# Optimization experiments

Measured on AMD Instinct MI355X. Metric: run time of the kernel, lower is better.

## Reference

```python
import jax, jax.numpy as jnp
import numpy as np

B, T, E, H, D = 4, 2048, 1024, 16, 64  # batch, seq(block_size), n_embed, num_heads, hidden_dim


def setup_inputs() -> dict:
    key = jax.random.key(0)
    ks = jax.random.split(key, 10)
    s_in = 1.0 / np.sqrt(E)
    return {
        "x": jax.random.normal(ks[0], (B, T, E), dtype=jnp.float32),
        "Wq": jax.random.normal(ks[1], (H, E, D), dtype=jnp.float32) * s_in,
        "bq": jnp.zeros((H, D), dtype=jnp.float32),
        "Wk": jax.random.normal(ks[2], (H, E, D), dtype=jnp.float32) * s_in,
        "bk": jnp.zeros((H, D), dtype=jnp.float32),
        "Wv": jax.random.normal(ks[3], (H, E, D), dtype=jnp.float32) * s_in,
        "bv": jnp.zeros((H, D), dtype=jnp.float32),
        "Wp": jax.random.normal(ks[4], (E, E), dtype=jnp.float32) * s_in,
        "bp": jnp.zeros((E,), dtype=jnp.float32),
    }


def reference(x, Wq, bq, Wk, bk, Wv, bv, Wp, bp):
    # Batched equivalent of the per-head Python loop: each head h computes
    # causal scaled-dot-product attention with its own Q/K/V projections.
    q = jnp.einsum("bte,hed->bhtd", x, Wq) + bq[None, :, None, :]
    k = jnp.einsum("bte,hed->bhtd", x, Wk) + bk[None, :, None, :]
    v = jnp.einsum("bte,hed->bhtd", x, Wv) + bv[None, :, None, :]
    scale = 1.0 / jnp.sqrt(jnp.asarray(D, dtype=x.dtype))
    scores = jnp.einsum("bhtd,bhsd->bhts", q, k) * scale  # [B,H,T,T]
    causal = jnp.tril(jnp.ones((T, T), dtype=bool))
    scores = jnp.where(causal[None, None, :, :], scores, jnp.asarray(-jnp.inf, dtype=x.dtype))
    att = jax.nn.softmax(scores, axis=-1)
    head_out = jnp.einsum("bhts,bhsd->bhtd", att, v)  # [B,H,T,D]
    # concat heads along last dim: [B,T,H*D] == [B,T,E]
    cat = head_out.transpose(0, 2, 1, 3).reshape(B, T, H * D)
    out = cat @ Wp + bp  # final projection (dropout is identity in eval)
    return out
```

## Files before the change

kernel.cpp:

```cpp
#include <hip/hip_runtime.h>


typedef __attribute__((ext_vector_type(8))) __bf16 bf16x8;
typedef __attribute__((ext_vector_type(4))) float f32x4;
typedef __attribute__((ext_vector_type(16))) float f32x16;
typedef __attribute__((ext_vector_type(4))) unsigned int u32x4;
typedef __attribute__((ext_vector_type(2))) unsigned int u32x2;
typedef unsigned short u16;
typedef unsigned int u32;

#define DEV __device__ __forceinline__

#define QK_SCALE 0.18033688011112042f

DEV u16 f2bf(float f) {
  u32 u = __builtin_bit_cast(u32, f);
  u += 0x7fffu + ((u >> 16) & 1u);
  return (u16)(u >> 16);
}
DEV u32 pack2(float a, float b) { return (u32)f2bf(a) | ((u32)f2bf(b) << 16); }

DEV float exp2_hw(float x) { float r; asm("v_exp_f32 %0, %1" : "=v"(r) : "v"(x)); return r; }
DEV u32 cvtpk_bf16(float lo, float hi) {
  u32 r; asm("v_cvt_pk_bf16_f32 %0, %1, %2" : "=v"(r) : "v"(lo), "v"(hi)); return r;
}
DEV void pl32swap(u32& a, u32& b) { asm("v_permlane32_swap_b32 %0, %1" : "+v"(a), "+v"(b)); }
DEV float max3f(float a, float b, float c) {
  float r; asm("v_max3_f32 %0, %1, %2, %3" : "=v"(r) : "v"(a), "v"(b), "v"(c)); return r;
}

DEV f32x16 zero16() { f32x16 z;
#pragma unroll
  for (int i = 0; i < 16; i++) z[i] = 0.f;
  return z; }

DEV void gll16(const u16* g, u16* l) {
  __builtin_amdgcn_global_load_lds((const __attribute__((address_space(1))) void*)g,
                                   (__attribute__((address_space(3))) void*)l, 16, 0, 0);
}

__global__ __launch_bounds__(256) void prep_all_kernel(
    const float* __restrict__ x, const float* __restrict__ bq, const float* __restrict__ bk,
    const float* __restrict__ bv, const float* __restrict__ Wq, const float* __restrict__ Wk,
    const float* __restrict__ Wv, const float* __restrict__ Wp,
    u16* __restrict__ xbf, float* __restrict__ bqkv, u16* __restrict__ wqkvT, u16* __restrict__ wpT) {
  __shared__ float t[64][65];
  int bidAll = blockIdx.x, tid = threadIdx.x;
  if (bidAll < 4096) {
    int gid = bidAll * 256 + tid;
    if (gid < 3072) {
      float v = (gid < 1024) ? bq[gid] * QK_SCALE : (gid < 2048 ? bk[gid - 1024] : bv[gid - 2048]);
      bqkv[gid] = v;
    }
    const float4* xv = (const float4*)x;
    float4 f0 = xv[(size_t)gid * 2];
    float4 f1 = xv[(size_t)gid * 2 + 1];
    u32x4 st;
    st.x = pack2(f0.x, f0.y); st.y = pack2(f0.z, f0.w);
    st.z = pack2(f1.x, f1.y); st.w = pack2(f1.z, f1.w);
    *(u32x4*)&xbf[(size_t)gid * 8] = st;
    return;
  }
  int bid = bidAll - 4096;
  int r0 = tid >> 6, c = tid & 63;
  if (bid < 768) {
    int p = bid >> 8, rem = bid & 255, h = rem >> 4, et = rem & 15;
    float sc = (p == 0) ? QK_SCALE : 1.0f;
    const float* src = (p == 0 ? Wq : (p == 1 ? Wk : Wv)) + ((size_t)h * 1024 + et * 64) * 64;
#pragma unroll
    for (int i = 0; i < 16; i++) { int e = r0 + i * 4; t[e][c] = src[(size_t)e * 64 + c]; }
    __syncthreads();
    u16* dst = wqkvT + ((size_t)p * 1024 + h * 64) * 1024 + et * 64;
#pragma unroll
    for (int i = 0; i < 16; i++) { int d = r0 + i * 4; dst[(size_t)d * 1024 + c] = f2bf(t[c][d] * sc); }
  } else {
    int b2 = bid - 768, rt = b2 >> 4, ct = b2 & 15;
#pragma unroll
    for (int i = 0; i < 16; i++) { int e = r0 + i * 4; t[e][c] = Wp[(size_t)(rt * 64 + e) * 1024 + ct * 64 + c]; }
    __syncthreads();
#pragma unroll
    for (int i = 0; i < 16; i++) { int f = r0 + i * 4; wpT[(size_t)(ct * 64 + f) * 1024 + rt * 64 + c] = f2bf(t[c][f]); }
  }
}

DEV void stage_tile32(const u16* __restrict__ X, int row0, int k0, u16* lds, int tid) {
#pragma unroll
  for (int j = 0; j < 2; j++) {
    int ci = j * 256 + tid;
    int L = ci >> 3, half = (ci >> 2) & 1, s = ci & 3;
    int row = L * 2 + half;
    int srcslot = s ^ (L & 3);
    gll16(X + (size_t)(row0 + row) * 1024 + k0 + srcslot * 8, lds + ci * 8);
  }
}

DEV int frag_off32(int row, int lg) {
  return (row >> 1) * 64 + (row & 1) * 32 + ((lg ^ ((row >> 1) & 3)) * 8);
}

__global__ __launch_bounds__(256, 4) void gemm128_kernel(
    const u16* __restrict__ A, const u16* __restrict__ Bt, const float* __restrict__ bias,
    int tilesN, int mode, u16* __restrict__ Qb, u16* __restrict__ Kb, u16* __restrict__ VTb,
    float* __restrict__ outF) {
  __shared__ u16 As[2][128 * 32];
  __shared__ u16 Bs[2][128 * 32];
  int nwg = gridDim.x;
  int bid = blockIdx.x;
  int swz = (bid % 8) * (nwg / 8) + bid / 8;
  int bm = swz / tilesN, bn = swz % tilesN;
  int tid = threadIdx.x;
  int lane = tid & 63, wave = tid >> 6;
  int wm = wave >> 1, wn = wave & 1;
  int lr = lane & 15, lg = lane >> 4;

  f32x4 acc[4][4];
#pragma unroll
  for (int i = 0; i < 4; i++)
#pragma unroll
    for (int j = 0; j < 4; j++) acc[i][j] = f32x4{0.f, 0.f, 0.f, 0.f};

  int aoff[4], boff[4];
#pragma unroll
  for (int i = 0; i < 4; i++) {
    aoff[i] = frag_off32(wm * 64 + i * 16 + lr, lg);
    boff[i] = frag_off32(wn * 64 + i * 16 + lr, lg);
  }

  stage_tile32(A, bm * 128, 0, As[0], tid);
  stage_tile32(Bt, bn * 128, 0, Bs[0], tid);
  __syncthreads();
  int cur = 0;

  for (int t = 0; t < 32; ++t) {
    if (t + 1 < 32) {
      stage_tile32(A, bm * 128, (t + 1) * 32, As[cur ^ 1], tid);
      stage_tile32(Bt, bn * 128, (t + 1) * 32, Bs[cur ^ 1], tid);
    }
    bf16x8 af[4], bfr[4];
#pragma unroll
    for (int i = 0; i < 4; i++) {
      af[i] = *(const bf16x8*)&As[cur][aoff[i]];
      bfr[i] = *(const bf16x8*)&Bs[cur][boff[i]];
    }
    __builtin_amdgcn_s_setprio(1);
#pragma unroll
    for (int i = 0; i < 4; i++)
#pragma unroll
      for (int j = 0; j < 4; j++)
        acc[i][j] = __builtin_amdgcn_mfma_f32_16x16x32_bf16(af[i], bfr[j], acc[i][j], 0, 0, 0);
    __builtin_amdgcn_s_setprio(0);
    __syncthreads();
    cur ^= 1;
  }

  int crow = bm * 128 + wm * 64;
  int ccol = bn * 128 + wn * 64;
  if (mode == 0) {
#pragma unroll
    for (int j = 0; j < 4; j++) {
      int col = ccol + j * 16 + lr;
      float bb = bias[col];
      int p = col >> 10, h = (col >> 6) & 15, d = col & 63;
#pragma unroll
      for (int i = 0; i < 4; i++) {
        int row0 = crow + i * 16 + lg * 4;
        int b_ = row0 >> 11, t0 = row0 & 2047;
        if (p == 2) {
          u32x2 pv;
          pv.x = pack2(acc[i][j][0] + bb, acc[i][j][1] + bb);
          pv.y = pack2(acc[i][j][2] + bb, acc[i][j][3] + bb);
          *(u32x2*)&VTb[((size_t)(b_ * 16 + h) * 64 + d) * 2048 + t0] = pv;
        } else {
          u16* dst = (p == 0 ? Qb : Kb);
#pragma unroll
          for (int r = 0; r < 4; r++)
            dst[((size_t)(b_ * 16 + h) * 2048 + (t0 + r)) * 64 + d] = f2bf(acc[i][j][r] + bb);
        }
      }
    }
  } else {
#pragma unroll
    for (int j = 0; j < 4; j++) {
      int col = ccol + j * 16 + lr;
      float bb = bias[col];
#pragma unroll
      for (int i = 0; i < 4; i++) {
        int row0 = crow + i * 16 + lg * 4;
#pragma unroll
        for (int r = 0; r < 4; r++)
          outF[(size_t)(row0 + r) * 1024 + col] = acc[i][j][r] + bb;
      }
    }
  }
}

DEV void stage_kv256(const u16* __restrict__ Kh, const u16* __restrict__ Vh, int kv0,
                     u16* Ksb, u16* Vsb, int tid) {
#pragma unroll
  for (int j = 0; j < 2; j++) {
    int ci = j * 256 + tid;
    int row = ci >> 3, slot = ci & 7;
    int ss = slot ^ (row & 7);
    __builtin_amdgcn_global_load_lds(
        (const __attribute__((address_space(1))) void*)(Kh + (size_t)(kv0 + row) * 64 + ss * 8),
        (__attribute__((address_space(3))) void*)(Ksb + ci * 8), 16, 0, 0);
    __builtin_amdgcn_global_load_lds(
        (const __attribute__((address_space(1))) void*)(Vh + (size_t)row * 2048 + kv0 + ss * 8),
        (__attribute__((address_space(3))) void*)(Vsb + ci * 8), 16, 0, 0);
  }
}

__global__ __launch_bounds__(256, 2) void attn_kernel(
    const u16* __restrict__ Qb, const u16* __restrict__ Kb, const u16* __restrict__ VTb,
    u16* __restrict__ cat) {
  __shared__ u16 Ks[2][64 * 64];
  __shared__ u16 Vs[2][64 * 64];
  int bid = blockIdx.x;
  int t = 15 - (bid >> 6);
  int bh = bid & 63;
  int b = bh >> 4, h = bh & 15;
  int tid = threadIdx.x, wave = tid >> 6, lane = tid & 63;
  int l31 = lane & 31, hi = lane >> 5;
  int q0w = t * 128 + wave * 32;
  int qrow = q0w + l31;

  const u16* Qh = Qb + (size_t)bh * 2048 * 64;
  const u16* Kh = Kb + (size_t)bh * 2048 * 64;
  const u16* Vh = VTb + (size_t)bh * 64 * 2048;

  bf16x8 qf[4];
#pragma unroll
  for (int ks = 0; ks < 4; ks++)
    qf[ks] = *(const bf16x8*)&Qh[(size_t)qrow * 64 + ks * 16 + hi * 8];

  u32 loff[4];
#pragma unroll
  for (int ks = 0; ks < 4; ks++)
    loff[ks] = (u32)(l31 * 128 + (((ks * 2 + hi) ^ (l31 & 7)) * 16));

  f32x16 o0 = zero16(), o1 = zero16();
  float m_run = -1e30f, l_run = 0.f;
  int iters = 2 * t + 2;

  stage_kv256(Kh, Vh, 0, Ks[0], Vs[0], tid);
  __syncthreads();
  int cur = 0;

  for (int kvt = 0; kvt < iters; ++kvt) {
    int kv0 = kvt * 64;
    if (kvt + 1 < iters) stage_kv256(Kh, Vh, kv0 + 64, Ks[cur ^ 1], Vs[cur ^ 1], tid);

    if (kv0 <= q0w + 31) {
      f32x16 s0 = zero16(), s1 = zero16();
      const char* kb = (const char*)&Ks[cur][0];
      __builtin_amdgcn_s_setprio(1);
#pragma unroll
      for (int ks = 0; ks < 4; ks++) {
        bf16x8 k0 = *(const bf16x8*)(kb + loff[ks]);
        bf16x8 k1 = *(const bf16x8*)(kb + loff[ks] + 4096);
        s0 = __builtin_amdgcn_mfma_f32_32x32x16_bf16(k0, qf[ks], s0, 0, 0, 0);
        s1 = __builtin_amdgcn_mfma_f32_32x32x16_bf16(k1, qf[ks], s1, 0, 0, 0);
      }
      __builtin_amdgcn_s_setprio(0);

      if (kv0 + 63 > q0w) {
        int relh = qrow - kv0 - 4 * hi;
#pragma unroll
        for (int r = 0; r < 16; r++) {
          int off = (r & 3) + 8 * (r >> 2);
          s0[r] = (off > relh) ? -1e30f : s0[r];
          s1[r] = (off + 32 > relh) ? -1e30f : s1[r];
        }
      }

      float ta = max3f(s0[0], s0[1], s0[2]);
      float tb = max3f(s0[4], s0[5], s0[6]);
      float tc = max3f(s0[8], s0[9], s0[10]);
      float td = max3f(s0[12], s0[13], s0[14]);
      ta = max3f(ta, s0[3], s1[0]);
      tb = max3f(tb, s0[7], s1[4]);
      tc = max3f(tc, s0[11], s1[8]);
      td = max3f(td, s0[15], s1[12]);
      ta = max3f(ta, s1[1], s1[2]);
      tb = max3f(tb, s1[5], s1[6]);
      tc = max3f(tc, s1[9], s1[10]);
      td = max3f(td, s1[13], s1[14]);
      ta = max3f(ta, s1[3], tb);
      tc = max3f(tc, s1[7], td);
      float tmax = max3f(ta, tc, s1[11]);
      tmax = fmaxf(tmax, s1[15]);
      tmax = fmaxf(tmax, __shfl_xor(tmax, 32));
      float corr = 1.f;
      if (!__all(tmax <= m_run + 8.f)) {
        float m_new = fmaxf(m_run, tmax);
        corr = exp2_hw(m_run - m_new);
        o0 = o0 * corr;
        o1 = o1 * corr;
        m_run = m_new;
      }
      float t0 = 0.f, t1 = 0.f, t2 = 0.f, t3 = 0.f;
#pragma unroll
      for (int j = 0; j < 4; j++) {
        float p00 = exp2_hw(s0[j * 4 + 0] - m_run); s0[j * 4 + 0] = p00; t0 += p00;
        float p01 = exp2_hw(s0[j * 4 + 1] - m_run); s0[j * 4 + 1] = p01; t1 += p01;
        float p02 = exp2_hw(s0[j * 4 + 2] - m_run); s0[j * 4 + 2] = p02; t2 += p02;
        float p03 = exp2_hw(s0[j * 4 + 3] - m_run); s0[j * 4 + 3] = p03; t3 += p03;
        float p10 = exp2_hw(s1[j * 4 + 0] - m_run); s1[j * 4 + 0] = p10; t0 += p10;
        float p11 = exp2_hw(s1[j * 4 + 1] - m_run); s1[j * 4 + 1] = p11; t1 += p11;
        float p12 = exp2_hw(s1[j * 4 + 2] - m_run); s1[j * 4 + 2] = p12; t2 += p12;
        float p13 = exp2_hw(s1[j * 4 + 3] - m_run); s1[j * 4 + 3] = p13; t3 += p13;
      }
      float ts = (t0 + t1) + (t2 + t3);
      ts += __shfl_xor(ts, 32);
      l_run = l_run * corr + ts;

      const char* vb = (const char*)&Vs[cur][0];
      __builtin_amdgcn_s_setprio(1);
#pragma unroll
      for (int ks = 0; ks < 4; ks++) {
        const f32x16& sb = (ks < 2) ? s0 : s1;
        int g2 = (ks & 1) * 8;
        u32 a  = cvtpk_bf16(sb[g2 + 0], sb[g2 + 1]);
        u32 c  = cvtpk_bf16(sb[g2 + 2], sb[g2 + 3]);
        u32 bb = cvtpk_bf16(sb[g2 + 4], sb[g2 + 5]);
        u32 d  = cvtpk_bf16(sb[g2 + 6], sb[g2 + 7]);
        pl32swap(a, bb);
        pl32swap(c, d);
        u32x4 wv; wv.x = a; wv.y = c; wv.z = bb; wv.w = d;
        bf16x8 pf = __builtin_bit_cast(bf16x8, wv);
        bf16x8 v0 = *(const bf16x8*)(vb + loff[ks]);
        bf16x8 v1 = *(const bf16x8*)(vb + loff[ks] + 4096);
        o0 = __builtin_amdgcn_mfma_f32_32x32x16_bf16(v0, pf, o0, 0, 0, 0);
        o1 = __builtin_amdgcn_mfma_f32_32x32x16_bf16(v1, pf, o1, 0, 0, 0);
      }
      __builtin_amdgcn_s_setprio(0);
    }

    __syncthreads();
    cur ^= 1;
  }

  float li = 1.0f / l_run;
#pragma unroll
  for (int m = 0; m < 8; m++) {
    int dbase = 2 * (m & 1) + 8 * (m >> 1) + 4 * hi;
    u32 w0 = cvtpk_bf16(o0[2 * m] * li, o0[2 * m + 1] * li);
    u32 w1 = cvtpk_bf16(o1[2 * m] * li, o1[2 * m + 1] * li);
    *(u32*)&cat[(size_t)(b * 2048 + qrow) * 1024 + h * 64 + dbase] = w0;
    *(u32*)&cat[(size_t)(b * 2048 + qrow) * 1024 + h * 64 + 32 + dbase] = w1;
  }
}

extern "C" void kernel_launch(void* const* d_in, const int* in_sizes, int n_in,
                              void* d_out, int out_size, void* d_ws, size_t ws_size,
                              hipStream_t stream) {
  const float* x  = (const float*)d_in[0];
  const float* Wq = (const float*)d_in[1];
  const float* bq = (const float*)d_in[2];
  const float* Wk = (const float*)d_in[3];
  const float* bk = (const float*)d_in[4];
  const float* Wv = (const float*)d_in[5];
  const float* bv = (const float*)d_in[6];
  const float* Wp = (const float*)d_in[7];
  const float* bp = (const float*)d_in[8];

  char* w = (char*)d_ws;
  u16* xbf    = (u16*)w;                 w += (size_t)8192 * 1024 * 2;
  u16* wqkvT  = (u16*)w;                 w += (size_t)3072 * 1024 * 2;
  u16* wpT    = (u16*)w;                 w += (size_t)1024 * 1024 * 2;
  float* bqkv = (float*)w;               w += (size_t)3072 * 4;
  u16* Qb     = (u16*)w;                 w += (size_t)64 * 2048 * 64 * 2;
  u16* Kb     = (u16*)w;                 w += (size_t)64 * 2048 * 64 * 2;
  u16* VTb    = (u16*)w;                 w += (size_t)64 * 64 * 2048 * 2;
  u16* cat    = (u16*)w;                 w += (size_t)8192 * 1024 * 2;

  prep_all_kernel<<<5120, 256, 0, stream>>>(x, bq, bk, bv, Wq, Wk, Wv, Wp, xbf, bqkv, wqkvT, wpT);
  gemm128_kernel<<<1536, 256, 0, stream>>>(xbf, wqkvT, bqkv, 24, 0, Qb, Kb, VTb, nullptr);
  attn_kernel<<<1024, 256, 0, stream>>>(Qb, Kb, VTb, cat);
  gemm128_kernel<<<512, 256, 0, stream>>>(cat, wpT, bp, 8, 1, nullptr, nullptr, nullptr, (float*)d_out);
}
```

Baseline: 160.6 us.

## Triple-buffer LDS staging in GEMM and attention with partial vmcnt waits

Both the projection GEMM and the attention kernel move from double to triple buffering of LDS tiles. They prefetch two tiles ahead and replace __syncthreads with an explicit s_waitcnt vmcnt(4) plus barrier, so the most recent prefetch can stay in flight across the barrier. The aim is to hide global-to-LDS load latency behind MFMA work. The cost is more LDS per block, and the GEMM launch bound drops from 4 to 3 blocks per CU, which may reduce occupancy.

New measurement: 158.7 us. No clear change (-1.1%).

```diff
diff --git a/kernel.cpp b/kernel.cpp
--- a/kernel.cpp
+++ b/kernel.cpp
@@ -38,6 +38,12 @@
   __builtin_amdgcn_global_load_lds((const __attribute__((address_space(1))) void*)g,
                                    (__attribute__((address_space(3))) void*)l, 16, 0, 0);
 }
+
+#define SCHEDB() __builtin_amdgcn_sched_barrier(0)
+#define FENCE4()  do { asm volatile("s_waitcnt vmcnt(4) lgkmcnt(0)" ::: "memory"); SCHEDB(); \
+                       __builtin_amdgcn_s_barrier(); SCHEDB(); } while (0)
+#define FENCE0()  do { asm volatile("s_waitcnt vmcnt(0) lgkmcnt(0)" ::: "memory"); SCHEDB(); \
+                       __builtin_amdgcn_s_barrier(); SCHEDB(); } while (0)
 
 __global__ __launch_bounds__(256) void prep_all_kernel(
     const float* __restrict__ x, const float* __restrict__ bq, const float* __restrict__ bk,
@@ -98,12 +104,12 @@
   return (row >> 1) * 64 + (row & 1) * 32 + ((lg ^ ((row >> 1) & 3)) * 8);
 }
 
-__global__ __launch_bounds__(256, 4) void gemm128_kernel(
+__global__ __launch_bounds__(256, 3) void gemm128_kernel(
     const u16* __restrict__ A, const u16* __restrict__ Bt, const float* __restrict__ bias,
     int tilesN, int mode, u16* __restrict__ Qb, u16* __restrict__ Kb, u16* __restrict__ VTb,
     float* __restrict__ outF) {
-  __shared__ u16 As[2][128 * 32];
-  __shared__ u16 Bs[2][128 * 32];
+  __shared__ u16 As[3][128 * 32];
+  __shared__ u16 Bs[3][128 * 32];
   int nwg = gridDim.x;
   int bid = blockIdx.x;
   int swz = (bid % 8) * (nwg / 8) + bid / 8;
@@ -128,19 +134,26 @@
 
   stage_tile32(A, bm * 128, 0, As[0], tid);
   stage_tile32(Bt, bn * 128, 0, Bs[0], tid);
-  __syncthreads();
-  int cur = 0;
-
+  stage_tile32(A, bm * 128, 32, As[1], tid);
+  stage_tile32(Bt, bn * 128, 32, Bs[1], tid);
+  asm volatile("s_waitcnt vmcnt(4)" ::: "memory");
+  SCHEDB();
+  __builtin_amdgcn_s_barrier();
+  SCHEDB();
+
+  int rs = 0;
   for (int t = 0; t < 32; ++t) {
-    if (t + 1 < 32) {
-      stage_tile32(A, bm * 128, (t + 1) * 32, As[cur ^ 1], tid);
-      stage_tile32(Bt, bn * 128, (t + 1) * 32, Bs[cur ^ 1], tid);
+    int ws = rs + 2; if (ws >= 3) ws -= 3;
+    bool st = (t + 2) < 32;
+    if (st) {
+      stage_tile32(A, bm * 128, (t + 2) * 32, As[ws], tid);
+      stage_tile32(Bt, bn * 128, (t + 2) * 32, Bs[ws], tid);
     }
     bf16x8 af[4], bfr[4];
 #pragma unroll
     for (int i = 0; i < 4; i++) {
-      af[i] = *(const bf16x8*)&As[cur][aoff[i]];
-      bfr[i] = *(const bf16x8*)&Bs[cur][boff[i]];
+      af[i] = *(const bf16x8*)&As[rs][aoff[i]];
+      bfr[i] = *(const bf16x8*)&Bs[rs][boff[i]];
     }
     __builtin_amdgcn_s_setprio(1);
 #pragma unroll
@@ -149,8 +162,8 @@
       for (int j = 0; j < 4; j++)
         acc[i][j] = __builtin_amdgcn_mfma_f32_16x16x32_bf16(af[i], bfr[j], acc[i][j], 0, 0, 0);
     __builtin_amdgcn_s_setprio(0);
-    __syncthreads();
-    cur ^= 1;
+    if (st) FENCE4(); else FENCE0();
+    rs = rs + 1; if (rs >= 3) rs -= 3;
   }
 
   int crow = bm * 128 + wm * 64;
@@ -201,20 +214,16 @@
     int ci = j * 256 + tid;
     int row = ci >> 3, slot = ci & 7;
     int ss = slot ^ (row & 7);
-    __builtin_amdgcn_global_load_lds(
-        (const __attribute__((address_space(1))) void*)(Kh + (size_t)(kv0 + row) * 64 + ss * 8),
-        (__attribute__((address_space(3))) void*)(Ksb + ci * 8), 16, 0, 0);
-    __builtin_amdgcn_global_load_lds(
-        (const __attribute__((address_space(1))) void*)(Vh + (size_t)row * 2048 + kv0 + ss * 8),
-        (__attribute__((address_space(3))) void*)(Vsb + ci * 8), 16, 0, 0);
+    gll16(Kh + (size_t)(kv0 + row) * 64 + ss * 8, Ksb + ci * 8);
+    gll16(Vh + (size_t)row * 2048 + kv0 + ss * 8, Vsb + ci * 8);
   }
 }
 
 __global__ __launch_bounds__(256, 2) void attn_kernel(
     const u16* __restrict__ Qb, const u16* __restrict__ Kb, const u16* __restrict__ VTb,
     u16* __restrict__ cat) {
-  __shared__ u16 Ks[2][64 * 64];
-  __shared__ u16 Vs[2][64 * 64];
+  __shared__ u16 Ks[3][64 * 64];
+  __shared__ u16 Vs[3][64 * 64];
   int bid = blockIdx.x;
   int t = 15 - (bid >> 6);
   int bh = bid & 63;
@@ -243,16 +252,22 @@
   int iters = 2 * t + 2;
 
   stage_kv256(Kh, Vh, 0, Ks[0], Vs[0], tid);
-  __syncthreads();
-  int cur = 0;
-
+  stage_kv256(Kh, Vh, 64, Ks[1], Vs[1], tid);
+  asm volatile("s_waitcnt vmcnt(4)" ::: "memory");
+  SCHEDB();
+  __builtin_amdgcn_s_barrier();
+  SCHEDB();
+
+  int rs = 0;
   for (int kvt = 0; kvt < iters; ++kvt) {
     int kv0 = kvt * 64;
-    if (kvt + 1 < iters) stage_kv256(Kh, Vh, kv0 + 64, Ks[cur ^ 1], Vs[cur ^ 1], tid);
+    int ws = rs + 2; if (ws >= 3) ws -= 3;
+    bool st = (kvt + 2) < iters;
+    if (st) stage_kv256(Kh, Vh, kv0 + 128, Ks[ws], Vs[ws], tid);
 
     if (kv0 <= q0w + 31) {
       f32x16 s0 = zero16(), s1 = zero16();
-      const char* kb = (const char*)&Ks[cur][0];
+      const char* kb = (const char*)&Ks[rs][0];
       __builtin_amdgcn_s_setprio(1);
 #pragma unroll
       for (int ks = 0; ks < 4; ks++) {
@@ -314,7 +329,7 @@
       ts += __shfl_xor(ts, 32);
       l_run = l_run * corr + ts;
 
-      const char* vb = (const char*)&Vs[cur][0];
+      const char* vb = (const char*)&Vs[rs][0];
       __builtin_amdgcn_s_setprio(1);
 #pragma unroll
       for (int ks = 0; ks < 4; ks++) {
@@ -336,8 +351,8 @@
       __builtin_amdgcn_s_setprio(0);
     }
 
-    __syncthreads();
-    cur ^= 1;
+    if (st) FENCE4(); else FENCE0();
+    rs = rs + 1; if (rs >= 3) rs -= 3;
   }
 
   float li = 1.0f / l_run;
```

## Switch projection GEMM to 32x32x16 MFMA with K=64 tiles

Applied to the files above, without the earlier changes.

The 128x128 projection GEMM now stages 64-wide K tiles instead of 32, halving the number of loop iterations and barriers. It also replaces the 16x16x32 MFMA with 32x32x16, which needs fewer LDS fragment loads per FLOP. The epilogue is rewritten for the 32x32 accumulator layout. LDS use doubles, so launch bounds drop from 4 to 2 blocks per CU, trading occupancy for reuse. The attention staging helper is switched to the shared gll16 wrapper, which is a cleanup only.

Result: slower. 166.0 us (+3.4%).

```diff
diff --git a/kernel.cpp b/kernel.cpp
--- a/kernel.cpp
+++ b/kernel.cpp
@@ -83,27 +83,22 @@
   }
 }
 
-DEV void stage_tile32(const u16* __restrict__ X, int row0, int k0, u16* lds, int tid) {
-#pragma unroll
-  for (int j = 0; j < 2; j++) {
+DEV void stage_tile(const u16* __restrict__ X, int row0, int k0, u16* lds, int tid) {
+#pragma unroll
+  for (int j = 0; j < 4; j++) {
     int ci = j * 256 + tid;
-    int L = ci >> 3, half = (ci >> 2) & 1, s = ci & 3;
-    int row = L * 2 + half;
-    int srcslot = s ^ (L & 3);
+    int row = ci >> 3, slot = ci & 7;
+    int srcslot = slot ^ (row & 7);
     gll16(X + (size_t)(row0 + row) * 1024 + k0 + srcslot * 8, lds + ci * 8);
   }
 }
 
-DEV int frag_off32(int row, int lg) {
-  return (row >> 1) * 64 + (row & 1) * 32 + ((lg ^ ((row >> 1) & 3)) * 8);
-}
-
-__global__ __launch_bounds__(256, 4) void gemm128_kernel(
+__global__ __launch_bounds__(256, 2) void gemm128_kernel(
     const u16* __restrict__ A, const u16* __restrict__ Bt, const float* __restrict__ bias,
     int tilesN, int mode, u16* __restrict__ Qb, u16* __restrict__ Kb, u16* __restrict__ VTb,
     float* __restrict__ outF) {
-  __shared__ u16 As[2][128 * 32];
-  __shared__ u16 Bs[2][128 * 32];
+  __shared__ u16 As[2][128 * 64];
+  __shared__ u16 Bs[2][128 * 64];
   int nwg = gridDim.x;
   int bid = blockIdx.x;
   int swz = (bid % 8) * (nwg / 8) + bid / 8;
@@ -111,84 +106,96 @@
   int tid = threadIdx.x;
   int lane = tid & 63, wave = tid >> 6;
   int wm = wave >> 1, wn = wave & 1;
-  int lr = lane & 15, lg = lane >> 4;
-
-  f32x4 acc[4][4];
-#pragma unroll
-  for (int i = 0; i < 4; i++)
-#pragma unroll
-    for (int j = 0; j < 4; j++) acc[i][j] = f32x4{0.f, 0.f, 0.f, 0.f};
-
-  int aoff[4], boff[4];
-#pragma unroll
-  for (int i = 0; i < 4; i++) {
-    aoff[i] = frag_off32(wm * 64 + i * 16 + lr, lg);
-    boff[i] = frag_off32(wn * 64 + i * 16 + lr, lg);
-  }
-
-  stage_tile32(A, bm * 128, 0, As[0], tid);
-  stage_tile32(Bt, bn * 128, 0, Bs[0], tid);
+  int l31 = lane & 31, hi = lane >> 5;
+
+  f32x16 acc[2][2];
+#pragma unroll
+  for (int i = 0; i < 2; i++)
+#pragma unroll
+    for (int j = 0; j < 2; j++) acc[i][j] = zero16();
+
+  int aoff[2][4], boff[2][4];
+#pragma unroll
+  for (int i = 0; i < 2; i++)
+#pragma unroll
+    for (int ks = 0; ks < 4; ks++) {
+      int ra = wm * 64 + i * 32 + l31;
+      aoff[i][ks] = ra * 64 + (((ks * 2 + hi) ^ (ra & 7)) * 8);
+      int rb = wn * 64 + i * 32 + l31;
+      boff[i][ks] = rb * 64 + (((ks * 2 + hi) ^ (rb & 7)) * 8);
+    }
+
+  stage_tile(A, bm * 128, 0, As[0], tid);
+  stage_tile(Bt, bn * 128, 0, Bs[0], tid);
   __syncthreads();
   int cur = 0;
 
-  for (int t = 0; t < 32; ++t) {
-    if (t + 1 < 32) {
-      stage_tile32(A, bm * 128, (t + 1) * 32, As[cur ^ 1], tid);
-      stage_tile32(Bt, bn * 128, (t + 1) * 32, Bs[cur ^ 1], tid);
-    }
-    bf16x8 af[4], bfr[4];
-#pragma unroll
-    for (int i = 0; i < 4; i++) {
-      af[i] = *(const bf16x8*)&As[cur][aoff[i]];
-      bfr[i] = *(const bf16x8*)&Bs[cur][boff[i]];
-    }
+  for (int t = 0; t < 16; ++t) {
+    if (t + 1 < 16) {
+      stage_tile(A, bm * 128, (t + 1) * 64, As[cur ^ 1], tid);
+      stage_tile(Bt, bn * 128, (t + 1) * 64, Bs[cur ^ 1], tid);
+    }
+    bf16x8 af[2][4], bfr[2][4];
+#pragma unroll
+    for (int i = 0; i < 2; i++)
+#pragma unroll
+      for (int ks = 0; ks < 4; ks++) {
+        af[i][ks] = *(const bf16x8*)&As[cur][aoff[i][ks]];
+        bfr[i][ks] = *(const bf16x8*)&Bs[cur][boff[i][ks]];
+      }
     __builtin_amdgcn_s_setprio(1);
 #pragma unroll
-    for (int i = 0; i < 4; i++)
-#pragma unroll
-      for (int j = 0; j < 4; j++)
-        acc[i][j] = __builtin_amdgcn_mfma_f32_16x16x32_bf16(af[i], bfr[j], acc[i][j], 0, 0, 0);
+    for (int ks = 0; ks < 4; ks++)
+#pragma unroll
+      for (int i = 0; i < 2; i++)
+#pragma unroll
+        for (int j = 0; j < 2; j++)
+          acc[i][j] = __builtin_amdgcn_mfma_f32_32x32x16_bf16(af[i][ks], bfr[j][ks], acc[i][j], 0, 0, 0);
     __builtin_amdgcn_s_setprio(0);
     __syncthreads();
     cur ^= 1;
   }
 
-  int crow = bm * 128 + wm * 64;
-  int ccol = bn * 128 + wn * 64;
   if (mode == 0) {
 #pragma unroll
-    for (int j = 0; j < 4; j++) {
-      int col = ccol + j * 16 + lr;
+    for (int j = 0; j < 2; j++) {
+      int col = bn * 128 + wn * 64 + j * 32 + l31;
       float bb = bias[col];
       int p = col >> 10, h = (col >> 6) & 15, d = col & 63;
 #pragma unroll
-      for (int i = 0; i < 4; i++) {
-        int row0 = crow + i * 16 + lg * 4;
-        int b_ = row0 >> 11, t0 = row0 & 2047;
-        if (p == 2) {
-          u32x2 pv;
-          pv.x = pack2(acc[i][j][0] + bb, acc[i][j][1] + bb);
-          pv.y = pack2(acc[i][j][2] + bb, acc[i][j][3] + bb);
-          *(u32x2*)&VTb[((size_t)(b_ * 16 + h) * 64 + d) * 2048 + t0] = pv;
-        } else {
-          u16* dst = (p == 0 ? Qb : Kb);
+      for (int i = 0; i < 2; i++) {
+        int rowb = bm * 128 + wm * 64 + i * 32 + 4 * hi;
+#pragma unroll
+        for (int rq = 0; rq < 4; rq++) {
+          int row0 = rowb + 8 * rq;
+          int b_ = row0 >> 11, t0 = row0 & 2047;
+          if (p == 2) {
+            u32x2 pv;
+            pv.x = pack2(acc[i][j][rq * 4 + 0] + bb, acc[i][j][rq * 4 + 1] + bb);
+            pv.y = pack2(acc[i][j][rq * 4 + 2] + bb, acc[i][j][rq * 4 + 3] + bb);
+            *(u32x2*)&VTb[((size_t)(b_ * 16 + h) * 64 + d) * 2048 + t0] = pv;
+          } else {
+            u16* dst = (p == 0 ? Qb : Kb);
+#pragma unroll
+            for (int r = 0; r < 4; r++)
+              dst[((size_t)(b_ * 16 + h) * 2048 + (t0 + r)) * 64 + d] = f2bf(acc[i][j][rq * 4 + r] + bb);
+          }
+        }
+      }
+    }
+  } else {
+#pragma unroll
+    for (int j = 0; j < 2; j++) {
+      int col = bn * 128 + wn * 64 + j * 32 + l31;
+      float bb = bias[col];
+#pragma unroll
+      for (int i = 0; i < 2; i++) {
+        int rowb = bm * 128 + wm * 64 + i * 32 + 4 * hi;
+#pragma unroll
+        for (int rq = 0; rq < 4; rq++)
 #pragma unroll
           for (int r = 0; r < 4; r++)
-            dst[((size_t)(b_ * 16 + h) * 2048 + (t0 + r)) * 64 + d] = f2bf(acc[i][j][r] + bb);
-        }
-      }
-    }
-  } else {
-#pragma unroll
-    for (int j = 0; j < 4; j++) {
-      int col = ccol + j * 16 + lr;
-      float bb = bias[col];
-#pragma unroll
-      for (int i = 0; i < 4; i++) {
-        int row0 = crow + i * 16 + lg * 4;
-#pragma unroll
-        for (int r = 0; r < 4; r++)
-          outF[(size_t)(row0 + r) * 1024 + col] = acc[i][j][r] + bb;
+            outF[(size_t)(rowb + 8 * rq + r) * 1024 + col] = acc[i][j][rq * 4 + r] + bb;
       }
     }
   }
@@ -201,12 +208,8 @@
     int ci = j * 256 + tid;
     int row = ci >> 3, slot = ci & 7;
     int ss = slot ^ (row & 7);
-    __builtin_amdgcn_global_load_lds(
-        (const __attribute__((address_space(1))) void*)(Kh + (size_t)(kv0 + row) * 64 + ss * 8),
-        (__attribute__((address_space(3))) void*)(Ksb + ci * 8), 16, 0, 0);
-    __builtin_amdgcn_global_load_lds(
-        (const __attribute__((address_space(1))) void*)(Vh + (size_t)row * 2048 + kv0 + ss * 8),
-        (__attribute__((address_space(3))) void*)(Vsb + ci * 8), 16, 0, 0);
+    gll16(Kh + (size_t)(kv0 + row) * 64 + ss * 8, Ksb + ci * 8);
+    gll16(Vh + (size_t)row * 2048 + kv0 + ss * 8, Vsb + ci * 8);
   }
 }
 
```
